# Optimization experiments

Hardware: AMD Instinct MI355X
Metric: run time of the kernel (lower is better)

## Reference

```python
import jax, jax.numpy as jnp
import numpy as np

B, S, D, E, L = 4, 384, 300, 50, 2
HD = D // L  # head_dim = 150


def _linear_params(k, fin, fout):
    bnd = 1.0 / np.sqrt(fin)
    kw, kb = jax.random.split(k)
    W = jax.random.uniform(kw, (fout, fin), minval=-bnd, maxval=bnd, dtype=jnp.float32)
    b = jax.random.uniform(kb, (fout,), minval=-bnd, maxval=bnd, dtype=jnp.float32)
    return W, b


def setup_inputs() -> dict:
    key = jax.random.key(0)
    ks = jax.random.split(key, 6)
    W0, b0 = _linear_params(ks[0], D, HD)            # weight_list[0]: Linear(300, 150)
    W1, b1 = _linear_params(ks[1], D + HD, HD)       # weight_list[1]: Linear(450, 150)
    Wh, bh = _linear_params(ks[2], 2 * HD + E, E)    # Edgeupdate.W: Linear(350, 50)
    Wout, bout = _linear_params(ks[3], D, D)         # linear_output: Linear(300, 300)
    adj = jax.random.uniform(ks[4], (B, S, S, E), dtype=jnp.float32)
    gcn_inputs = jax.random.normal(ks[5], (B, S, D), dtype=jnp.float32)
    return dict(adj=adj, gcn_inputs=gcn_inputs, W0=W0, b0=b0, W1=W1, b1=b1,
                Wh=Wh, bh=bh, Wout=Wout, bout=bout)


def reference(adj, gcn_inputs, W0, b0, W1, b1, Wh, bh, Wout, bout):
    # Edgeupdate weight split: cat order is [edge(E), node1(HD), node2(HD)]
    Wh_e = Wh[:, :E]            # [E, E]
    Wh_1 = Wh[:, E:E + HD]      # [E, HD]
    Wh_2 = Wh[:, E + HD:]       # [E, HD]

    outputs = gcn_inputs        # [B, S, D]
    cache = [gcn_inputs]
    out_list = []
    for (Wl, bl) in ((W0, b0), (W1, b1)):
        e_dim = adj.shape[-1]
        # mean over edge channels of (adj_e @ outputs): einsum fuses the mean
        Ax = jnp.einsum('bike,bkd->bid', adj, outputs) / e_dim   # [B, S, din]
        # AxW = W_l(Ax) + W_l(outputs)  (same linear applied twice, bias twice)
        AxW = (Ax @ Wl.T + bl) + (outputs @ Wl.T + bl)           # [B, S, HD]
        gAxW = jax.nn.relu(AxW)
        # Edgeupdate highway: new_edge[b,i,j] = W([edge[b,i,j]; g[b,j]; g[b,i]]) + bh
        # (node1[b,i,j] = g[b,j], node2[b,i,j] = g[b,i] from the expand/permute)
        edge_part = adj @ Wh_e.T                                  # [B, S, S, E]
        n1 = gAxW @ Wh_1.T                                        # [B, S, E]
        n2 = gAxW @ Wh_2.T                                        # [B, S, E]
        adj = edge_part + n1[:, None, :, :] + n2[:, :, None, :] + bh
        cache.append(gAxW)
        outputs = jnp.concatenate(cache, axis=2)                  # growing concat
        out_list.append(gAxW)  # gcn_drop is identity in eval mode

    gcn_outputs = jnp.concatenate(out_list, axis=2) + gcn_inputs  # [B, S, D]
    return gcn_outputs @ Wout.T + bout
```

## Files before the change

kernel.cpp:

```cpp
#include <hip/hip_runtime.h>

constexpr int Bc  = 4;
constexpr int Sc  = 384;
constexpr int Dc  = 300;
constexpr int Ec  = 50;
constexpr int HDc = 150;
constexpr int WHC = 350;

typedef __attribute__((ext_vector_type(8))) short bf16x8;
typedef __attribute__((ext_vector_type(4))) float f32x4;

__device__ __forceinline__ short f2bf(float x) {
    union { float f; unsigned u; } v; v.f = x;
    unsigned r = (v.u + 0x7FFFu + ((v.u >> 16) & 1u)) >> 16;
    return (short)r;
}

__global__ void prep_kernel(const float* __restrict__ Wh,
                            const float* __restrict__ bh,
                            float* __restrict__ sm) {
    int t = threadIdx.x;
    if (t < Ec) {
        float s = 0.f;
        for (int e = 0; e < Ec; ++e) s += Wh[e*WHC + t];
        sm[t] = s;
    } else if (t >= 64 && t < 64 + HDc) {
        int h = t - 64;
        float s = 0.f;
        for (int e = 0; e < Ec; ++e) s += Wh[e*WHC + Ec + h];
        sm[t] = s;
    } else if (t >= 224 && t < 224 + HDc) {
        int h = t - 224;
        float s = 0.f;
        for (int e = 0; e < Ec; ++e) s += Wh[e*WHC + Ec + HDc + h];
        sm[t] = s;
    } else if (t == 384) {
        float s = 0.f;
        for (int e = 0; e < Ec; ++e) s += bh[e];
        sm[t] = s;
    }
}

__global__ __launch_bounds__(256)
void reduce_adj2(const float* __restrict__ adj, const float* __restrict__ sm,
                 float* __restrict__ A0, float* __restrict__ wadj) {
    __shared__ float wec[64];
    __shared__ float tile[256 * 51];
    int t = threadIdx.x;
    if (t < Ec) wec[t] = sm[t];
    long base = (long)blockIdx.x * (256 * 50);
    const float4* p4 = (const float4*)(adj + base);
    for (int i = t; i < 3200; i += 256) {
        float4 v = p4[i];
        int e = 4 * i;
        tile[(e/50)*51 + (e%50)]         = v.x;
        tile[((e+1)/50)*51 + ((e+1)%50)] = v.y;
        tile[((e+2)/50)*51 + ((e+2)%50)] = v.z;
        tile[((e+3)/50)*51 + ((e+3)%50)] = v.w;
    }
    __syncthreads();
    const float* row = tile + t * 51;
    float s = 0.f, w = 0.f;
    #pragma unroll
    for (int i = 0; i < 50; ++i) { float v = row[i]; s += v; w += v * wec[i]; }
    int r = blockIdx.x * 256 + t;
    A0[r]   = s * (1.0f / Ec);
    wadj[r] = w;
}

template<int BSRC, int A1M, int HASD, int HASB, int RELU>
__global__ __launch_bounds__(256)
void mgemm(const float* __restrict__ A, int lda, long sA,
           const float* __restrict__ Bw, int ldb, long sB,
           const float* __restrict__ W1a, const float* __restrict__ WoutP,
           const float* __restrict__ Dm, int ldd, long sD,
           const float* __restrict__ bias, float bscale,
           const float* __restrict__ s12, const float* __restrict__ sm,
           float* __restrict__ C, int ldc, long sC,
           int M, int N, int K)
{
    const int b = blockIdx.z;
    const float* Ap = A + (long)b * sA;
    const float* Bp = Bw + (long)b * sB;
    const float* Dp = Dm + (long)b * sD;
    float* Cp = C + (long)b * sC;

    __shared__ short As[32 * 40];
    __shared__ short Bs[32 * 40];

    const int tid  = threadIdx.x;
    const int wave = tid >> 6, lane = tid & 63;
    const int wm = wave & 1, wn = wave >> 1;
    const int lm = lane & 15, quad = lane >> 4;
    const int m0 = blockIdx.y * 32, n0 = blockIdx.x * 32;

    const int srow = tid >> 3;
    const int sk   = (tid & 7) * 4;
    const int nc   = tid & 31;
    const int kr   = tid >> 5;

    float sbh = 0.f; const float* s1p = nullptr; float s2v = 0.f;
    if constexpr (A1M) {
        sbh = sm[384];
        s1p = s12 + 2L * Sc * b;
        s2v = s1p[2 * (m0 + srow) + 1];
    }

    float ra[4], rb[4];

    auto stageA = [&](int k0) {
        int am = m0 + srow;
        int kb = k0 + sk;
        if constexpr (A1M) {
            float4 v = *(const float4*)(Ap + (long)am * lda + kb);
            const float* vp = (const float*)&v;
            #pragma unroll
            for (int j = 0; j < 4; ++j)
                ra[j] = (vp[j] + s1p[2 * (kb + j)] + s2v + sbh) * (1.0f / Ec);
        } else {
            if (kb + 3 < K) {
                float4 v = *(const float4*)(Ap + (long)am * lda + kb);
                ra[0] = v.x; ra[1] = v.y; ra[2] = v.z; ra[3] = v.w;
            } else {
                #pragma unroll
                for (int j = 0; j < 4; ++j) {
                    int k = kb + j;
                    ra[j] = (k < K) ? Ap[(long)am * lda + k] : 0.f;
                }
            }
        }
    };

    auto stageB = [&](int k0) {
        if constexpr (BSRC == 0) {
            int n = n0 + nc;
            bool nok = n < N;
            #pragma unroll
            for (int p = 0; p < 4; ++p) {
                int k = k0 + kr + p * 8;
                rb[p] = (nok && k < K) ? Bp[(long)k * ldb + n] : 0.f;
            }
        } else {
            int nr = n0 + srow;
            bool nok = nr < N;
            const float* wp = Bp; int ld = ldb; int nn = nr;
            if constexpr (BSRC == 2) {
                if (nr < 150)      { wp = Bp;    ld = 300; nn = nr; }
                else if (nr < 300) { wp = W1a;   ld = 450; nn = nr - 150; }
                else               { wp = WoutP; ld = 300; nn = nr - 300; }
            }
            #pragma unroll
            for (int p = 0; p < 2; ++p) {
                int k = k0 + sk + 2 * p;
                if (nok && k + 1 < K) {
                    float2 v = *(const float2*)(wp + (long)nn * ld + k);
                    rb[2*p] = v.x; rb[2*p + 1] = v.y;
                } else {
                    rb[2*p]     = (nok && k < K)     ? wp[(long)nn * ld + k]     : 0.f;
                    rb[2*p + 1] = (nok && k + 1 < K) ? wp[(long)nn * ld + k + 1] : 0.f;
                }
            }
        }
    };

    auto stash = [&]() {
        #pragma unroll
        for (int j = 0; j < 4; ++j) As[srow * 40 + sk + j] = f2bf(ra[j]);
        if constexpr (BSRC == 0) {
            #pragma unroll
            for (int p = 0; p < 4; ++p) Bs[nc * 40 + kr + p * 8] = f2bf(rb[p]);
        } else {
            #pragma unroll
            for (int j = 0; j < 4; ++j) Bs[srow * 40 + sk + j] = f2bf(rb[j]);
        }
    };

    f32x4 acc = {0.f, 0.f, 0.f, 0.f};

    stageA(0); stageB(0);
    for (int k0 = 0; k0 < K; k0 += 32) {
        __syncthreads();
        stash();
        __syncthreads();
        if (k0 + 32 < K) { stageA(k0 + 32); stageB(k0 + 32); }
        bf16x8 af  = *(const bf16x8*)(As + (wm * 16 + lm) * 40 + quad * 8);
        bf16x8 bfv = *(const bf16x8*)(Bs + (wn * 16 + lm) * 40 + quad * 8);
        acc = __builtin_amdgcn_mfma_f32_16x16x32_bf16(af, bfv, acc, 0, 0, 0);
    }

    int cn = n0 + wn * 16 + lm;
    if (cn < N) {
        #pragma unroll
        for (int r = 0; r < 4; ++r) {
            int cm = m0 + wm * 16 + quad * 4 + r;
            if (cm < M) {
                float v = acc[r];
                if constexpr (HASD) v += Dp[(long)cm * ldd + cn];
                if constexpr (HASB) v += bscale * bias[cn];
                if constexpr (RELU) v = fmaxf(v, 0.f);
                Cp[(long)cm * ldc + cn] = v;
            }
        }
    }
}

__global__ __launch_bounds__(256)
void s12k(const float* __restrict__ G, const float* __restrict__ sm,
          float* __restrict__ s12) {
    int wave = threadIdx.x >> 6, lane = threadIdx.x & 63;
    int g = blockIdx.x * 4 + wave;
    const float* gp = G + (long)g * Dc;
    float a = 0.f, c = 0.f;
    #pragma unroll
    for (int h0 = 0; h0 < HDc; h0 += 64) {
        int h = h0 + lane;
        if (h < HDc) { float v = gp[h]; a += v * sm[64 + h]; c += v * sm[224 + h]; }
    }
    #pragma unroll
    for (int off = 32; off; off >>= 1) {
        a += __shfl_down(a, off);
        c += __shfl_down(c, off);
    }
    if (lane == 0) { s12[2*g] = a; s12[2*g + 1] = c; }
}

extern "C" void kernel_launch(void* const* d_in, const int* in_sizes, int n_in,
                              void* d_out, int out_size, void* d_ws, size_t ws_size,
                              hipStream_t stream) {
    const float* adj  = (const float*)d_in[0];
    const float* X    = (const float*)d_in[1];
    const float* W0   = (const float*)d_in[2];
    const float* b0   = (const float*)d_in[3];
    const float* W1   = (const float*)d_in[4];
    const float* b1   = (const float*)d_in[5];
    const float* Wh   = (const float*)d_in[6];
    const float* bh   = (const float*)d_in[7];
    const float* Wout = (const float*)d_in[8];
    const float* bout = (const float*)d_in[9];
    float* out = (float*)d_out;

    float* ws   = (float*)d_ws;
    float* sm   = ws;
    float* A0   = sm + 512;
    float* wadj = A0 + Bc * Sc * Sc;
    float* R    = wadj + Bc * Sc * Sc;
    float* Gbuf = R + (long)Bc * Sc * 600;
    float* s12  = Gbuf + (long)Bc * Sc * Dc;

    const int MT = Bc * Sc;
    const long AS = (long)Sc * Sc;
    const long RS = (long)Sc * 600;
    const long GS = (long)Sc * Dc;

    prep_kernel<<<1, 512, 0, stream>>>(Wh, bh, sm);

    reduce_adj2<<<(Bc*Sc*Sc) / 256, 256, 0, stream>>>(adj, sm, A0, wadj);

    mgemm<2,0,0,0,0><<<dim3(19, 48, 1), 256, 0, stream>>>(
        X, Dc, 0, W0, 300, 0, W1, Wout,
        nullptr, 0, 0, nullptr, 0.f, nullptr, nullptr,
        R, 600, 0, MT, 600, Dc);

    mgemm<0,0,1,1,1><<<dim3(5, 12, Bc), 256, 0, stream>>>(
        A0, Sc, AS, R, 600, RS, nullptr, nullptr,
        R, 600, RS, b0, 2.0f, nullptr, nullptr,
        Gbuf, Dc, GS, Sc, HDc, Sc);

    s12k<<<MT / 4, 256, 0, stream>>>(Gbuf, sm, s12);

    mgemm<1,0,1,0,0><<<dim3(5, 48, 1), 256, 0, stream>>>(
        Gbuf, Dc, 0, W1 + Dc, Dc + HDc, 0, nullptr, nullptr,
        R + HDc, 600, 0, nullptr, 0.f, nullptr, nullptr,
        R + HDc, 600, 0, MT, HDc, HDc);

    mgemm<0,1,1,1,1><<<dim3(5, 12, Bc), 256, 0, stream>>>(
        wadj, Sc, AS, R + HDc, 600, RS, nullptr, nullptr,
        R + HDc, 600, RS, b1, 2.0f, s12, sm,
        Gbuf + HDc, Dc, GS, Sc, HDc, Sc);

    mgemm<1,0,1,1,0><<<dim3(10, 48, 1), 256, 0, stream>>>(
        Gbuf, Dc, 0, Wout, Dc, 0, nullptr, nullptr,
        R + 2*HDc, 600, 0, bout, 1.0f, nullptr, nullptr,
        out, Dc, 0, MT, Dc, Dc);
}
```

Before: 261.1 us.

## Shrink adj reduction tiles and double the GEMM K-step to 64

The adj reduction kernel now handles 64 rows per block, using four threads per row and shuffle reductions. This cuts shared memory from about 52KB to 13KB so more blocks fit per CU, and loads are issued up front. The GEMM kernel stages 64 K-elements per iteration and issues two MFMAs per sync, halving the barrier count. The BSRC==0 path drops its k<K guard, which risks reading past K when K is not a multiple of 64 (K=384 is fine here).

```diff
diff --git a/kernel.cpp b/kernel.cpp
--- a/kernel.cpp
+++ b/kernel.cpp
@@ -42,30 +42,47 @@
 }
 
 __global__ __launch_bounds__(256)
-void reduce_adj2(const float* __restrict__ adj, const float* __restrict__ sm,
+void reduce_adj3(const float* __restrict__ adj, const float* __restrict__ sm,
                  float* __restrict__ A0, float* __restrict__ wadj) {
+    __shared__ float tile[64 * 51];
     __shared__ float wec[64];
-    __shared__ float tile[256 * 51];
     int t = threadIdx.x;
     if (t < Ec) wec[t] = sm[t];
-    long base = (long)blockIdx.x * (256 * 50);
+
+    long base = (long)blockIdx.x * 3200;
     const float4* p4 = (const float4*)(adj + base);
-    for (int i = t; i < 3200; i += 256) {
-        float4 v = p4[i];
-        int e = 4 * i;
-        tile[(e/50)*51 + (e%50)]         = v.x;
-        tile[((e+1)/50)*51 + ((e+1)%50)] = v.y;
-        tile[((e+2)/50)*51 + ((e+2)%50)] = v.z;
-        tile[((e+3)/50)*51 + ((e+3)%50)] = v.w;
-    }
+    float4 v0 = p4[t];
+    float4 v1 = p4[t + 256];
+    float4 v2 = p4[t + 512];
+    float4 v3 = {0.f, 0.f, 0.f, 0.f};
+    if (t < 32) v3 = p4[t + 768];
+
+    auto scat = [&](int i, const float4& v) {
+        const float* vp = (const float*)&v;
+        #pragma unroll
+        for (int j = 0; j < 4; ++j) {
+            int e = 4 * i + j;
+            tile[(e / 50) * 51 + (e % 50)] = vp[j];
+        }
+    };
+    scat(t, v0);
+    scat(t + 256, v1);
+    scat(t + 512, v2);
+    if (t < 32) scat(t + 768, v3);
     __syncthreads();
-    const float* row = tile + t * 51;
+
+    int r = t >> 2, q = t & 3;
+    int h0 = q * 13, h1 = (q == 3) ? 50 : h0 + 13;
+    const float* row = tile + r * 51;
     float s = 0.f, w = 0.f;
-    #pragma unroll
-    for (int i = 0; i < 50; ++i) { float v = row[i]; s += v; w += v * wec[i]; }
-    int r = blockIdx.x * 256 + t;
-    A0[r]   = s * (1.0f / Ec);
-    wadj[r] = w;
+    for (int i = h0; i < h1; ++i) { float v = row[i]; s += v; w += v * wec[i]; }
+    s += __shfl_xor(s, 1); w += __shfl_xor(w, 1);
+    s += __shfl_xor(s, 2); w += __shfl_xor(w, 2);
+    if (q == 0) {
+        int g = blockIdx.x * 64 + r;
+        A0[g]   = s * (1.0f / Ec);
+        wadj[g] = w;
+    }
 }
 
 template<int BSRC, int A1M, int HASD, int HASB, int RELU>
@@ -85,8 +102,8 @@
     const float* Dp = Dm + (long)b * sD;
     float* Cp = C + (long)b * sC;
 
-    __shared__ short As[32 * 40];
-    __shared__ short Bs[32 * 40];
+    __shared__ short As[32 * 72];
+    __shared__ short Bs[32 * 72];
 
     const int tid  = threadIdx.x;
     const int wave = tid >> 6, lane = tid & 63;
@@ -95,7 +112,7 @@
     const int m0 = blockIdx.y * 32, n0 = blockIdx.x * 32;
 
     const int srow = tid >> 3;
-    const int sk   = (tid & 7) * 4;
+    const int sk   = (tid & 7) * 8;
     const int nc   = tid & 31;
     const int kr   = tid >> 5;
 
@@ -106,24 +123,30 @@
         s2v = s1p[2 * (m0 + srow) + 1];
     }
 
-    float ra[4], rb[4];
+    float ra[8], rb[8];
 
     auto stageA = [&](int k0) {
         int am = m0 + srow;
         int kb = k0 + sk;
         if constexpr (A1M) {
-            float4 v = *(const float4*)(Ap + (long)am * lda + kb);
-            const float* vp = (const float*)&v;
-            #pragma unroll
-            for (int j = 0; j < 4; ++j)
-                ra[j] = (vp[j] + s1p[2 * (kb + j)] + s2v + sbh) * (1.0f / Ec);
+            float4 u = *(const float4*)(Ap + (long)am * lda + kb);
+            float4 w = *(const float4*)(Ap + (long)am * lda + kb + 4);
+            const float* up = (const float*)&u;
+            const float* wp = (const float*)&w;
+            #pragma unroll
+            for (int j = 0; j < 4; ++j) {
+                ra[j]     = (up[j] + s1p[2*(kb + j)]     + s2v + sbh) * (1.0f/Ec);
+                ra[4 + j] = (wp[j] + s1p[2*(kb + 4 + j)] + s2v + sbh) * (1.0f/Ec);
+            }
         } else {
-            if (kb + 3 < K) {
-                float4 v = *(const float4*)(Ap + (long)am * lda + kb);
-                ra[0] = v.x; ra[1] = v.y; ra[2] = v.z; ra[3] = v.w;
+            if (kb + 7 < K) {
+                float4 u = *(const float4*)(Ap + (long)am * lda + kb);
+                float4 w = *(const float4*)(Ap + (long)am * lda + kb + 4);
+                ra[0]=u.x; ra[1]=u.y; ra[2]=u.z; ra[3]=u.w;
+                ra[4]=w.x; ra[5]=w.y; ra[6]=w.z; ra[7]=w.w;
             } else {
                 #pragma unroll
-                for (int j = 0; j < 4; ++j) {
+                for (int j = 0; j < 8; ++j) {
                     int k = kb + j;
                     ra[j] = (k < K) ? Ap[(long)am * lda + k] : 0.f;
                 }
@@ -136,9 +159,9 @@
             int n = n0 + nc;
             bool nok = n < N;
             #pragma unroll
-            for (int p = 0; p < 4; ++p) {
+            for (int p = 0; p < 8; ++p) {
                 int k = k0 + kr + p * 8;
-                rb[p] = (nok && k < K) ? Bp[(long)k * ldb + n] : 0.f;
+                rb[p] = nok ? Bp[(long)k * ldb + n] : 0.f;
             }
         } else {
             int nr = n0 + srow;
@@ -150,7 +173,7 @@
                 else               { wp = WoutP; ld = 300; nn = nr - 300; }
             }
             #pragma unroll
-            for (int p = 0; p < 2; ++p) {
+            for (int p = 0; p < 4; ++p) {
                 int k = k0 + sk + 2 * p;
                 if (nok && k + 1 < K) {
                     float2 v = *(const float2*)(wp + (long)nn * ld + k);
@@ -165,27 +188,32 @@
 
     auto stash = [&]() {
         #pragma unroll
-        for (int j = 0; j < 4; ++j) As[srow * 40 + sk + j] = f2bf(ra[j]);
+        for (int j = 0; j < 8; ++j) As[srow * 72 + sk + j] = f2bf(ra[j]);
         if constexpr (BSRC == 0) {
             #pragma unroll
-            for (int p = 0; p < 4; ++p) Bs[nc * 40 + kr + p * 8] = f2bf(rb[p]);
+            for (int p = 0; p < 8; ++p) Bs[nc * 72 + kr + p * 8] = f2bf(rb[p]);
         } else {
             #pragma unroll
-            for (int j = 0; j < 4; ++j) Bs[srow * 40 + sk + j] = f2bf(rb[j]);
+            for (int j = 0; j < 8; ++j) Bs[srow * 72 + sk + j] = f2bf(rb[j]);
         }
     };
 
     f32x4 acc = {0.f, 0.f, 0.f, 0.f};
 
     stageA(0); stageB(0);
-    for (int k0 = 0; k0 < K; k0 += 32) {
+    for (int k0 = 0; k0 < K; k0 += 64) {
         __syncthreads();
         stash();
         __syncthreads();
-        if (k0 + 32 < K) { stageA(k0 + 32); stageB(k0 + 32); }
-        bf16x8 af  = *(const bf16x8*)(As + (wm * 16 + lm) * 40 + quad * 8);
-        bf16x8 bfv = *(const bf16x8*)(Bs + (wn * 16 + lm) * 40 + quad * 8);
-        acc = __builtin_amdgcn_mfma_f32_16x16x32_bf16(af, bfv, acc, 0, 0, 0);
+        if (k0 + 64 < K) { stageA(k0 + 64); stageB(k0 + 64); }
+        {
+            bf16x8 a0 = *(const bf16x8*)(As + (wm*16 + lm) * 72 + quad * 8);
+            bf16x8 b0 = *(const bf16x8*)(Bs + (wn*16 + lm) * 72 + quad * 8);
+            acc = __builtin_amdgcn_mfma_f32_16x16x32_bf16(a0, b0, acc, 0, 0, 0);
+            bf16x8 a1 = *(const bf16x8*)(As + (wm*16 + lm) * 72 + 32 + quad * 8);
+            bf16x8 b1 = *(const bf16x8*)(Bs + (wn*16 + lm) * 72 + 32 + quad * 8);
+            acc = __builtin_amdgcn_mfma_f32_16x16x32_bf16(a1, b1, acc, 0, 0, 0);
+        }
     }
 
     int cn = n0 + wn * 16 + lm;
@@ -254,7 +282,7 @@
 
     prep_kernel<<<1, 512, 0, stream>>>(Wh, bh, sm);
 
-    reduce_adj2<<<(Bc*Sc*Sc) / 256, 256, 0, stream>>>(adj, sm, A0, wadj);
+    reduce_adj3<<<(Bc*Sc*Sc) / 64, 256, 0, stream>>>(adj, sm, A0, wadj);
 
     mgemm<2,0,0,0,0><<<dim3(19, 48, 1), 256, 0, stream>>>(
         X, Dc, 0, W0, 300, 0, W1, Wout,
```

Measured after the change: 244.6 us. -6.3%, faster.
